# Performance work log

Measured on AMD Instinct MI355X. Metric: run time of the kernel, lower is better.

The kernel has to match this reference:

```python
import jax, jax.numpy as jnp
import numpy as np

D = 1024  # input_dim

def setup_inputs() -> dict:
    key = jax.random.key(0)
    ks = jax.random.split(key, 7)
    s = 1.0 / np.sqrt(D)
    x = jax.random.normal(ks[0], (8, 2048, D), dtype=jnp.float32)
    Wq = jax.random.uniform(ks[1], (D, D), jnp.float32, -s, s)
    bq = jax.random.uniform(ks[2], (D,), jnp.float32, -s, s)
    Wk = jax.random.uniform(ks[3], (D, D), jnp.float32, -s, s)
    bk = jax.random.uniform(ks[4], (D,), jnp.float32, -s, s)
    Wv = jax.random.uniform(ks[5], (D, D), jnp.float32, -s, s)
    bv = jax.random.uniform(ks[6], (D,), jnp.float32, -s, s)
    return {"x": x, "Wq": Wq, "bq": bq, "Wk": Wk, "bk": bk, "Wv": Wv, "bv": bv}

def reference(x, Wq, bq, Wk, bk, Wv, bv):
    # torch.nn.Linear: y = x @ W.T + b
    q = jnp.einsum('bsd,ed->bse', x, Wq) + bq
    k = jnp.einsum('bsd,ed->bse', x, Wk) + bk
    v = jnp.einsum('bsd,ed->bse', x, Wv) + bv
    scores = jnp.einsum('bqd,bkd->bqk', q, k) / jnp.sqrt(jnp.float32(x.shape[-1]))
    attn = jax.nn.softmax(scores, axis=2)
    return jnp.einsum('bqk,bkd->bqd', attn, v)
```

## Files before the change

### kernel.cpp

```cpp
#include <hip/hip_runtime.h>
#include <stdint.h>


typedef __bf16 bf16_t;
typedef __bf16 bf16x8 __attribute__((ext_vector_type(8)));
typedef __bf16 bf16x4 __attribute__((ext_vector_type(4)));
typedef float f32x4 __attribute__((ext_vector_type(4)));

__device__ __forceinline__ void gload_lds16(const bf16_t* g, bf16_t* l) {
    __builtin_amdgcn_global_load_lds((const __attribute__((address_space(1))) void*)g,
                                     (__attribute__((address_space(3))) void*)l,
                                     16, 0, 0);
}

template <int EPI, int LDA, int LDB>
__device__ __forceinline__ void gemm_bt_core(
    const bf16_t* __restrict__ A,
    const bf16_t* __restrict__ B,
    bf16_t* __restrict__ Cb, float* __restrict__ Cf, int ldc,
    float* __restrict__ aux, float scale, int K,
    int m0, int n0)
{
    __shared__ bf16_t smem[128 * 136];
    bf16_t* As = smem;
    bf16_t* Bs = smem + 8192;

    const int t    = threadIdx.x;
    const int lane = t & 63;
    const int wave = t >> 6;
    const int wm   = wave >> 1;
    const int wn   = wave & 1;
    const int lr   = lane & 15;
    const int quad = lane >> 4;
    const int swz  = lr & 7;

    const int srow   = t >> 3;
    const int schunk = ((t & 7) ^ (srow & 7)) * 8;

    f32x4 acc[4][4];
#pragma unroll
    for (int i = 0; i < 4; i++)
#pragma unroll
        for (int j = 0; j < 4; j++) acc[i][j] = (f32x4){0.f, 0.f, 0.f, 0.f};

    const bf16_t* Ag = A + (size_t)(m0 + srow) * LDA + schunk;
    const bf16_t* Bg = B + (size_t)(n0 + srow) * LDB + schunk;

    for (int kt = 0; kt < K; kt += 64) {
#pragma unroll
        for (int j = 0; j < 4; j++) {
            gload_lds16(Ag + (size_t)j * 32 * LDA + kt, As + j * 2048 + t * 8);
            gload_lds16(Bg + (size_t)j * 32 * LDB + kt, Bs + j * 2048 + t * 8);
        }
        __syncthreads();

#pragma unroll
        for (int s = 0; s < 2; s++) {
            const int koff = ((s * 4 + quad) ^ swz) * 8;
            bf16x8 af[4], bfr[4];
#pragma unroll
            for (int i = 0; i < 4; i++)
                af[i] = *(const bf16x8*)(As + (wm * 64 + i * 16 + lr) * 64 + koff);
#pragma unroll
            for (int j = 0; j < 4; j++)
                bfr[j] = *(const bf16x8*)(Bs + (wn * 64 + j * 16 + lr) * 64 + koff);
#pragma unroll
            for (int i = 0; i < 4; i++)
#pragma unroll
                for (int j = 0; j < 4; j++)
                    acc[i][j] = __builtin_amdgcn_mfma_f32_16x16x32_bf16(af[i], bfr[j], acc[i][j], 0, 0, 0);
        }
        __syncthreads();
    }

    if (EPI == 0 || EPI == 1) {
#pragma unroll
        for (int j = 0; j < 4; j++) {
            const int col = wn * 64 + j * 16 + lr;
            const float bv = (EPI == 0) ? aux[n0 + col] : 0.f;
#pragma unroll
            for (int i = 0; i < 4; i++) {
                const int row = wm * 64 + i * 16 + quad * 4;
#pragma unroll
                for (int r = 0; r < 4; r++) {
                    float v = (EPI == 0) ? (acc[i][j][r] + bv)
                                         : __expf(acc[i][j][r] * scale);
                    smem[(row + r) * 136 + col] = (__bf16)v;
                }
            }
        }
        __syncthreads();
        const int lr2  = t >> 1;
        const int half = t & 1;
        float part = 0.f;
#pragma unroll
        for (int c8 = 0; c8 < 8; c8++) {
            const int col0 = half * 64 + c8 * 8;
            bf16x8 v = *(const bf16x8*)(smem + lr2 * 136 + col0);
            *(bf16x8*)(Cb + (size_t)(m0 + lr2) * ldc + n0 + col0) = v;
            if (EPI == 1) {
#pragma unroll
                for (int e = 0; e < 8; e++) part += (float)v[e];
            }
        }
        if (EPI == 1) {
            part += __shfl_xor(part, 1);
            if (half == 0) atomicAdd(aux + m0 + lr2, part);
        }
    } else if (EPI == 2) {
#pragma unroll
        for (int i = 0; i < 4; i++) {
            const int row = m0 + wm * 64 + i * 16 + quad * 4;
#pragma unroll
            for (int r = 0; r < 4; r++) {
                const float s = 1.0f / aux[row + r];
                float* crow = Cf + (size_t)(row + r) * ldc + n0 + wn * 64 + lr;
#pragma unroll
                for (int j = 0; j < 4; j++)
                    crow[j * 16] = acc[i][j][r] * s;
            }
        }
    } else {
#pragma unroll
        for (int j = 0; j < 4; j++) {
            const int col = n0 + wn * 64 + j * 16 + lr;
            const float bv = aux[col];
#pragma unroll
            for (int i = 0; i < 4; i++) {
                const int rowg = m0 + wm * 64 + i * 16 + quad * 4;
                const int b    = rowg >> 11;
                const int s    = rowg & 2047;
                bf16x4 p = { (__bf16)(acc[i][j][0] + bv), (__bf16)(acc[i][j][1] + bv),
                             (__bf16)(acc[i][j][2] + bv), (__bf16)(acc[i][j][3] + bv) };
                *(bf16x4*)(Cb + ((size_t)b << 21) + ((size_t)col << 11) + s) = p;
            }
        }
    }
}


__global__ __launch_bounds__(256) void k_qkv3(
    const bf16_t* __restrict__ xb, const bf16_t* __restrict__ Wb,
    bf16_t* __restrict__ Q, bf16_t* __restrict__ Vt,
    const float* __restrict__ bq, const float* __restrict__ bk,
    const float* __restrict__ bv)
{
    const int lid  = blockIdx.x + 8 * blockIdx.y + 1024 * blockIdx.z;
    const int xcd  = lid & 7;
    const int slot = lid >> 3;
    const int z    = slot >> 7;
    const int rem  = slot & 127;
    const int xt   = rem & 7;
    const int yt   = xcd * 16 + (rem >> 3);
    if (z < 2) {
        float* bias = (float*)((z == 0) ? bq : bk);
        gemm_bt_core<0, 1024, 1024>(xb, Wb + (size_t)z * 1048576,
                                    Q + (size_t)z * 16777216, nullptr, 1024,
                                    bias, 0.f, 1024, yt * 128, xt * 128);
    } else {
        gemm_bt_core<3, 1024, 1024>(xb, Wb + (size_t)2 * 1048576,
                                    Vt, nullptr, 0,
                                    (float*)bv, 0.f, 1024, yt * 128, xt * 128);
    }
}

__global__ __launch_bounds__(256) void k_scores(
    const bf16_t* __restrict__ Q, const bf16_t* __restrict__ Km,
    bf16_t* __restrict__ U, float* __restrict__ l)
{
    const int lid = blockIdx.x + 16 * blockIdx.y + 256 * blockIdx.z;
    const int b   = lid & 7;
    const int si  = lid >> 3;
    const int xt  = si & 15;
    const int yt  = si >> 4;
    gemm_bt_core<1, 1024, 1024>(Q + (size_t)b * 2048 * 1024,
                                Km + (size_t)b * 2048 * 1024,
                                U + (size_t)b * 2048 * 2048, nullptr, 2048,
                                l + b * 2048, 0.03125f, 1024,
                                yt * 128, xt * 128);
}

__global__ __launch_bounds__(256) void k_pv(
    const bf16_t* __restrict__ U, const bf16_t* __restrict__ Vt,
    float* __restrict__ Out, float* __restrict__ l)
{
    const int lid = blockIdx.x + 8 * blockIdx.y + 128 * blockIdx.z;
    const int b   = lid & 7;
    const int si  = lid >> 3;
    const int xt  = si & 7;
    const int yt  = si >> 3;
    gemm_bt_core<2, 2048, 2048>(U + (size_t)b * 2048 * 2048,
                                Vt + (size_t)b * 1024 * 2048,
                                nullptr, Out + (size_t)b * 2048 * 1024, 1024,
                                l + b * 2048, 0.f, 2048,
                                yt * 128, xt * 128);
}

__global__ __launch_bounds__(256) void k_cvt(
    const float* __restrict__ in, bf16_t* __restrict__ out, long ngroups,
    float* __restrict__ l)
{
    long idx    = (long)blockIdx.x * blockDim.x + threadIdx.x;
    long stride = (long)gridDim.x * blockDim.x;
    if (blockIdx.x < 64) l[blockIdx.x * 256 + threadIdx.x] = 0.f;
    for (long i = idx; i < ngroups; i += stride) {
        float4 v = ((const float4*)in)[i];
        bf16x4 o = { (__bf16)v.x, (__bf16)v.y, (__bf16)v.z, (__bf16)v.w };
        ((bf16x4*)out)[i] = o;
    }
}

__global__ __launch_bounds__(256) void k_cvt3(
    const float* __restrict__ w0, const float* __restrict__ w1,
    const float* __restrict__ w2, bf16_t* __restrict__ out)
{
    const int z = blockIdx.z;
    const float* in = (z == 0) ? w0 : (z == 1) ? w1 : w2;
    bf16_t* o = out + (size_t)z * 1048576;
    long i = (long)blockIdx.x * blockDim.x + threadIdx.x;
    float4 v = ((const float4*)in)[i];
    bf16x4 ov = { (__bf16)v.x, (__bf16)v.y, (__bf16)v.z, (__bf16)v.w };
    ((bf16x4*)o)[i] = ov;
}


extern "C" void kernel_launch(void* const* d_in, const int* in_sizes, int n_in,
                              void* d_out, int out_size, void* d_ws, size_t ws_size,
                              hipStream_t stream)
{
    const float* x  = (const float*)d_in[0];
    const float* Wq = (const float*)d_in[1];
    const float* bq = (const float*)d_in[2];
    const float* Wk = (const float*)d_in[3];
    const float* bk = (const float*)d_in[4];
    const float* Wv = (const float*)d_in[5];
    const float* bv = (const float*)d_in[6];

    bf16_t* Q    = (bf16_t*)d_ws;
    bf16_t* Km   = Q + 16777216;
    bf16_t* Vt   = Km + 16777216;
    bf16_t* U    = Vt + 16777216;
    bf16_t* xb   = U;
    bf16_t* Wb   = U + 33554432;
    float*  l    = (float*)(Wb + 3145728);

    k_cvt<<<dim3(2048), 256, 0, stream>>>(x, xb, 16777216 / 4, l);
    k_cvt3<<<dim3(1024, 1, 3), 256, 0, stream>>>(Wq, Wk, Wv, Wb);
    k_qkv3<<<dim3(8, 128, 3), 256, 0, stream>>>(xb, Wb, Q, Vt, bq, bk, bv);
    k_scores<<<dim3(16, 16, 8), 256, 0, stream>>>(Q, Km, U, l);
    k_pv<<<dim3(8, 16, 8), 256, 0, stream>>>(U, Vt, (float*)d_out, l);
}
```

Baseline: 440.5 us.

## Switch GEMMs to 256x256 tiles with 4-stage LDS pipeline and 8 waves

Replaces the 128x128 single-buffered GEMM core with a 256x256 tile computed by 512 threads (8 waves, each owning 128x64). A 4-slot LDS ring with K-step 32 keeps three tiles of global_load_lds in flight, using explicit vmcnt waits, split barriers and setprio so MFMA work overlaps the loads. The epilogues are adapted to stage the output in two halves, and the grids are reshaped to match. The aim is more data reuse per loaded byte and hidden memory latency, at the cost of one block per CU, 128 KB of LDS, and fewer blocks to balance across the CUs.

```diff
diff --git a/kernel.cpp b/kernel.cpp
--- a/kernel.cpp
+++ b/kernel.cpp
@@ -14,120 +14,162 @@
 }
 
 template <int EPI, int LDA, int LDB>
-__device__ __forceinline__ void gemm_bt_core(
+__device__ __forceinline__ void gemm256_core(
+    bf16_t* __restrict__ lds,
     const bf16_t* __restrict__ A,
     const bf16_t* __restrict__ B,
     bf16_t* __restrict__ Cb, float* __restrict__ Cf, int ldc,
     float* __restrict__ aux, float scale, int K,
     int m0, int n0)
 {
-    __shared__ bf16_t smem[128 * 136];
-    bf16_t* As = smem;
-    bf16_t* Bs = smem + 8192;
-
     const int t    = threadIdx.x;
     const int lane = t & 63;
     const int wave = t >> 6;
-    const int wm   = wave >> 1;
-    const int wn   = wave & 1;
+    const int wm   = wave >> 2;
+    const int wn   = wave & 3;
     const int lr   = lane & 15;
     const int quad = lane >> 4;
-    const int swz  = lr & 7;
-
-    const int srow   = t >> 3;
-    const int schunk = ((t & 7) ^ (srow & 7)) * 8;
-
-    f32x4 acc[4][4];
-#pragma unroll
-    for (int i = 0; i < 4; i++)
+
+    const int rowS = t >> 2;
+    const int qS   = (t & 3) ^ (rowS & 3);
+    const bf16_t* Ag = A + (size_t)(m0 + rowS) * LDA + qS * 8;
+    const bf16_t* Bg = B + (size_t)(n0 + rowS) * LDB + qS * 8;
+    const int dst0 = t * 8;
+
+    const int ko   = (quad ^ (lr & 3)) * 8;
+    const int aoff = (wm * 128 + lr) * 32 + ko;
+    const int boff = (wn * 64 + lr) * 32 + ko;
+
+    f32x4 acc[8][4];
+#pragma unroll
+    for (int i = 0; i < 8; i++)
 #pragma unroll
         for (int j = 0; j < 4; j++) acc[i][j] = (f32x4){0.f, 0.f, 0.f, 0.f};
 
-    const bf16_t* Ag = A + (size_t)(m0 + srow) * LDA + schunk;
-    const bf16_t* Bg = B + (size_t)(n0 + srow) * LDB + schunk;
-
-    for (int kt = 0; kt < K; kt += 64) {
-#pragma unroll
-        for (int j = 0; j < 4; j++) {
-            gload_lds16(Ag + (size_t)j * 32 * LDA + kt, As + j * 2048 + t * 8);
-            gload_lds16(Bg + (size_t)j * 32 * LDB + kt, Bs + j * 2048 + t * 8);
-        }
-        __syncthreads();
-
-#pragma unroll
-        for (int s = 0; s < 2; s++) {
-            const int koff = ((s * 4 + quad) ^ swz) * 8;
-            bf16x8 af[4], bfr[4];
-#pragma unroll
-            for (int i = 0; i < 4; i++)
-                af[i] = *(const bf16x8*)(As + (wm * 64 + i * 16 + lr) * 64 + koff);
-#pragma unroll
-            for (int j = 0; j < 4; j++)
-                bfr[j] = *(const bf16x8*)(Bs + (wn * 64 + j * 16 + lr) * 64 + koff);
-#pragma unroll
-            for (int i = 0; i < 4; i++)
-#pragma unroll
-                for (int j = 0; j < 4; j++)
-                    acc[i][j] = __builtin_amdgcn_mfma_f32_16x16x32_bf16(af[i], bfr[j], acc[i][j], 0, 0, 0);
-        }
-        __syncthreads();
+    const int T = K >> 5;
+
+#pragma unroll
+    for (int tt = 0; tt < 3; ++tt) {
+        bf16_t* Ab = lds + tt * 16384;
+        bf16_t* Bb = Ab + 8192;
+        const int kt = tt * 32;
+        gload_lds16(Ag + kt,                     Ab + dst0);
+        gload_lds16(Ag + kt + (size_t)128 * LDA, Ab + 4096 + dst0);
+        gload_lds16(Bg + kt,                     Bb + dst0);
+        gload_lds16(Bg + kt + (size_t)128 * LDB, Bb + 4096 + dst0);
+    }
+    asm volatile("s_waitcnt vmcnt(8)" ::: "memory");
+    __builtin_amdgcn_s_barrier();
+    __builtin_amdgcn_sched_barrier(0);
+
+    for (int tk = 0; tk < T; ++tk) {
+        const bf16_t* Ab = lds + (tk & 3) * 16384;
+        const bf16_t* Bb = Ab + 8192;
+        bf16x8 af[8], bfr[4];
+#pragma unroll
+        for (int i = 0; i < 4; ++i)
+            af[i] = *(const bf16x8*)(Ab + aoff + 512 * i);
+#pragma unroll
+        for (int j = 0; j < 4; ++j)
+            bfr[j] = *(const bf16x8*)(Bb + boff + 512 * j);
+        __builtin_amdgcn_s_barrier();
+        __builtin_amdgcn_sched_barrier(0);
+        __builtin_amdgcn_s_setprio(1);
+#pragma unroll
+        for (int i = 0; i < 4; ++i)
+#pragma unroll
+            for (int j = 0; j < 4; ++j)
+                acc[i][j] = __builtin_amdgcn_mfma_f32_16x16x32_bf16(af[i], bfr[j], acc[i][j], 0, 0, 0);
+        __builtin_amdgcn_s_setprio(0);
+#pragma unroll
+        for (int i = 4; i < 8; ++i)
+            af[i] = *(const bf16x8*)(Ab + aoff + 512 * i);
+        if (tk + 3 < T) {
+            bf16_t* An = lds + ((tk + 3) & 3) * 16384;
+            bf16_t* Bn = An + 8192;
+            const int kt = (tk + 3) * 32;
+            gload_lds16(Ag + kt,                     An + dst0);
+            gload_lds16(Ag + kt + (size_t)128 * LDA, An + 4096 + dst0);
+            gload_lds16(Bg + kt,                     Bn + dst0);
+            gload_lds16(Bg + kt + (size_t)128 * LDB, Bn + 4096 + dst0);
+            asm volatile("s_waitcnt vmcnt(8)" ::: "memory");
+        } else if (tk + 2 < T) {
+            asm volatile("s_waitcnt vmcnt(4)" ::: "memory");
+        } else {
+            asm volatile("s_waitcnt vmcnt(0)" ::: "memory");
+        }
+        __builtin_amdgcn_s_barrier();
+        __builtin_amdgcn_sched_barrier(0);
+        __builtin_amdgcn_s_setprio(1);
+#pragma unroll
+        for (int i = 4; i < 8; ++i)
+#pragma unroll
+            for (int j = 0; j < 4; ++j)
+                acc[i][j] = __builtin_amdgcn_mfma_f32_16x16x32_bf16(af[i], bfr[j], acc[i][j], 0, 0, 0);
+        __builtin_amdgcn_s_setprio(0);
     }
 
     if (EPI == 0 || EPI == 1) {
 #pragma unroll
-        for (int j = 0; j < 4; j++) {
-            const int col = wn * 64 + j * 16 + lr;
-            const float bv = (EPI == 0) ? aux[n0 + col] : 0.f;
-#pragma unroll
-            for (int i = 0; i < 4; i++) {
-                const int row = wm * 64 + i * 16 + quad * 4;
-#pragma unroll
-                for (int r = 0; r < 4; r++) {
-                    float v = (EPI == 0) ? (acc[i][j][r] + bv)
-                                         : __expf(acc[i][j][r] * scale);
-                    smem[(row + r) * 136 + col] = (__bf16)v;
+        for (int h = 0; h < 2; ++h) {
+            __syncthreads();
+            if (wm == h) {
+#pragma unroll
+                for (int j = 0; j < 4; ++j) {
+                    const int col = wn * 64 + j * 16 + lr;
+                    const float bv = (EPI == 0) ? aux[n0 + col] : 0.f;
+#pragma unroll
+                    for (int i = 0; i < 8; ++i) {
+                        const int row = i * 16 + quad * 4;
+#pragma unroll
+                        for (int r = 0; r < 4; ++r) {
+                            float v = (EPI == 0) ? (acc[i][j][r] + bv)
+                                                 : __expf(acc[i][j][r] * scale);
+                            lds[(row + r) * 264 + col] = (__bf16)v;
+                        }
+                    }
                 }
             }
-        }
-        __syncthreads();
-        const int lr2  = t >> 1;
-        const int half = t & 1;
-        float part = 0.f;
-#pragma unroll
-        for (int c8 = 0; c8 < 8; c8++) {
-            const int col0 = half * 64 + c8 * 8;
-            bf16x8 v = *(const bf16x8*)(smem + lr2 * 136 + col0);
-            *(bf16x8*)(Cb + (size_t)(m0 + lr2) * ldc + n0 + col0) = v;
+            __syncthreads();
+            const int r2 = t >> 2;
+            const int c0 = (t & 3) * 8;
+            float part = 0.f;
+#pragma unroll
+            for (int c = 0; c < 8; ++c) {
+                bf16x8 v = *(const bf16x8*)(lds + r2 * 264 + c0 + c * 32);
+                *(bf16x8*)(Cb + (size_t)(m0 + h * 128 + r2) * ldc + n0 + c0 + c * 32) = v;
+                if (EPI == 1) {
+#pragma unroll
+                    for (int e = 0; e < 8; ++e) part += (float)v[e];
+                }
+            }
             if (EPI == 1) {
-#pragma unroll
-                for (int e = 0; e < 8; e++) part += (float)v[e];
-            }
-        }
-        if (EPI == 1) {
-            part += __shfl_xor(part, 1);
-            if (half == 0) atomicAdd(aux + m0 + lr2, part);
+                part += __shfl_xor(part, 1);
+                part += __shfl_xor(part, 2);
+                if ((t & 3) == 0) atomicAdd(aux + m0 + h * 128 + r2, part);
+            }
         }
     } else if (EPI == 2) {
 #pragma unroll
-        for (int i = 0; i < 4; i++) {
-            const int row = m0 + wm * 64 + i * 16 + quad * 4;
-#pragma unroll
-            for (int r = 0; r < 4; r++) {
-                const float s = 1.0f / aux[row + r];
-                float* crow = Cf + (size_t)(row + r) * ldc + n0 + wn * 64 + lr;
-#pragma unroll
-                for (int j = 0; j < 4; j++)
+        for (int i = 0; i < 8; ++i) {
+            const int rowb = m0 + wm * 128 + i * 16 + quad * 4;
+#pragma unroll
+            for (int r = 0; r < 4; ++r) {
+                const float s = 1.0f / aux[rowb + r];
+                float* crow = Cf + (size_t)(rowb + r) * ldc + n0 + wn * 64 + lr;
+#pragma unroll
+                for (int j = 0; j < 4; ++j)
                     crow[j * 16] = acc[i][j][r] * s;
             }
         }
     } else {
 #pragma unroll
-        for (int j = 0; j < 4; j++) {
+        for (int j = 0; j < 4; ++j) {
             const int col = n0 + wn * 64 + j * 16 + lr;
             const float bv = aux[col];
 #pragma unroll
-            for (int i = 0; i < 4; i++) {
-                const int rowg = m0 + wm * 64 + i * 16 + quad * 4;
+            for (int i = 0; i < 8; ++i) {
+                const int rowg = m0 + wm * 128 + i * 16 + quad * 4;
                 const int b    = rowg >> 11;
                 const int s    = rowg & 2047;
                 bf16x4 p = { (__bf16)(acc[i][j][0] + bv), (__bf16)(acc[i][j][1] + bv),
@@ -139,61 +181,64 @@
 }
 
 
-__global__ __launch_bounds__(256) void k_qkv3(
+__global__ __launch_bounds__(512, 1) void k_qkv3(
     const bf16_t* __restrict__ xb, const bf16_t* __restrict__ Wb,
     bf16_t* __restrict__ Q, bf16_t* __restrict__ Vt,
     const float* __restrict__ bq, const float* __restrict__ bk,
     const float* __restrict__ bv)
 {
-    const int lid  = blockIdx.x + 8 * blockIdx.y + 1024 * blockIdx.z;
+    __shared__ bf16_t lds[65536];
+    const int lid  = blockIdx.x + 8 * blockIdx.y;
     const int xcd  = lid & 7;
     const int slot = lid >> 3;
-    const int z    = slot >> 7;
-    const int rem  = slot & 127;
-    const int xt   = rem & 7;
-    const int yt   = xcd * 16 + (rem >> 3);
+    const int z    = slot >> 5;
+    const int rem  = slot & 31;
+    const int xt   = rem & 3;
+    const int yt   = xcd * 8 + (rem >> 2);
     if (z < 2) {
         float* bias = (float*)((z == 0) ? bq : bk);
-        gemm_bt_core<0, 1024, 1024>(xb, Wb + (size_t)z * 1048576,
+        gemm256_core<0, 1024, 1024>(lds, xb, Wb + (size_t)z * 1048576,
                                     Q + (size_t)z * 16777216, nullptr, 1024,
-                                    bias, 0.f, 1024, yt * 128, xt * 128);
+                                    bias, 0.f, 1024, yt * 256, xt * 256);
     } else {
-        gemm_bt_core<3, 1024, 1024>(xb, Wb + (size_t)2 * 1048576,
+        gemm256_core<3, 1024, 1024>(lds, xb, Wb + (size_t)2 * 1048576,
                                     Vt, nullptr, 0,
-                                    (float*)bv, 0.f, 1024, yt * 128, xt * 128);
-    }
-}
-
-__global__ __launch_bounds__(256) void k_scores(
+                                    (float*)bv, 0.f, 1024, yt * 256, xt * 256);
+    }
+}
+
+__global__ __launch_bounds__(512, 1) void k_scores(
     const bf16_t* __restrict__ Q, const bf16_t* __restrict__ Km,
     bf16_t* __restrict__ U, float* __restrict__ l)
 {
-    const int lid = blockIdx.x + 16 * blockIdx.y + 256 * blockIdx.z;
-    const int b   = lid & 7;
-    const int si  = lid >> 3;
-    const int xt  = si & 15;
-    const int yt  = si >> 4;
-    gemm_bt_core<1, 1024, 1024>(Q + (size_t)b * 2048 * 1024,
-                                Km + (size_t)b * 2048 * 1024,
-                                U + (size_t)b * 2048 * 2048, nullptr, 2048,
-                                l + b * 2048, 0.03125f, 1024,
-                                yt * 128, xt * 128);
-}
-
-__global__ __launch_bounds__(256) void k_pv(
-    const bf16_t* __restrict__ U, const bf16_t* __restrict__ Vt,
-    float* __restrict__ Out, float* __restrict__ l)
-{
-    const int lid = blockIdx.x + 8 * blockIdx.y + 128 * blockIdx.z;
+    __shared__ bf16_t lds[65536];
+    const int lid = blockIdx.x + 8 * blockIdx.y;
     const int b   = lid & 7;
     const int si  = lid >> 3;
     const int xt  = si & 7;
     const int yt  = si >> 3;
-    gemm_bt_core<2, 2048, 2048>(U + (size_t)b * 2048 * 2048,
+    gemm256_core<1, 1024, 1024>(lds, Q + (size_t)b * 2048 * 1024,
+                                Km + (size_t)b * 2048 * 1024,
+                                U + (size_t)b * 2048 * 2048, nullptr, 2048,
+                                l + b * 2048, 0.03125f, 1024,
+                                yt * 256, xt * 256);
+}
+
+__global__ __launch_bounds__(512, 1) void k_pv(
+    const bf16_t* __restrict__ U, const bf16_t* __restrict__ Vt,
+    float* __restrict__ Out, float* __restrict__ l)
+{
+    __shared__ bf16_t lds[65536];
+    const int lid = blockIdx.x + 8 * blockIdx.y;
+    const int b   = lid & 7;
+    const int si  = lid >> 3;
+    const int xt  = si & 3;
+    const int yt  = si >> 2;
+    gemm256_core<2, 2048, 2048>(lds, U + (size_t)b * 2048 * 2048,
                                 Vt + (size_t)b * 1024 * 2048,
                                 nullptr, Out + (size_t)b * 2048 * 1024, 1024,
                                 l + b * 2048, 0.f, 2048,
-                                yt * 128, xt * 128);
+                                yt * 256, xt * 256);
 }
 
 __global__ __launch_bounds__(256) void k_cvt(
@@ -246,7 +291,7 @@
 
     k_cvt<<<dim3(2048), 256, 0, stream>>>(x, xb, 16777216 / 4, l);
     k_cvt3<<<dim3(1024, 1, 3), 256, 0, stream>>>(Wq, Wk, Wv, Wb);
-    k_qkv3<<<dim3(8, 128, 3), 256, 0, stream>>>(xb, Wb, Q, Vt, bq, bk, bv);
-    k_scores<<<dim3(16, 16, 8), 256, 0, stream>>>(Q, Km, U, l);
-    k_pv<<<dim3(8, 16, 8), 256, 0, stream>>>(U, Vt, (float*)d_out, l);
-}
+    k_qkv3<<<dim3(8, 96), 512, 0, stream>>>(xb, Wb, Q, Vt, bq, bk, bv);
+    k_scores<<<dim3(8, 64), 512, 0, stream>>>(Q, Km, U, l);
+    k_pv<<<dim3(8, 32), 512, 0, stream>>>(U, Vt, (float*)d_out, l);
+}
```

New measurement: 383.7 us. 12.9% less time.

## Triple-buffer GEMM K-loop with async LDS prefetch and split MFMA phases

Applied to the files above, without the earlier changes.

Replaces the single-buffered 64-wide K loop, which synchronized twice per step, with a three-stage ring of 32-wide K tiles in LDS. Global-to-LDS loads for step tk+2 are issued while the current tile is computed, and vmcnt waits plus raw s_barrier split each step into two MFMA halves. The change also adds s_setprio around the MFMA bursts, a new XOR swizzle for the 32-wide tiles, and launch_bounds(256,2) to request two blocks per CU. The price is more LDS (48KB per block) and fragile hand-written wait counts and barriers.

```diff
diff --git a/kernel.cpp b/kernel.cpp
--- a/kernel.cpp
+++ b/kernel.cpp
@@ -15,16 +15,13 @@
 
 template <int EPI, int LDA, int LDB>
 __device__ __forceinline__ void gemm_bt_core(
+    bf16_t* __restrict__ lds,
     const bf16_t* __restrict__ A,
     const bf16_t* __restrict__ B,
     bf16_t* __restrict__ Cb, float* __restrict__ Cf, int ldc,
     float* __restrict__ aux, float scale, int K,
     int m0, int n0)
 {
-    __shared__ bf16_t smem[128 * 136];
-    bf16_t* As = smem;
-    bf16_t* Bs = smem + 8192;
-
     const int t    = threadIdx.x;
     const int lane = t & 63;
     const int wave = t >> 6;
@@ -32,10 +29,16 @@
     const int wn   = wave & 1;
     const int lr   = lane & 15;
     const int quad = lane >> 4;
-    const int swz  = lr & 7;
-
-    const int srow   = t >> 3;
-    const int schunk = ((t & 7) ^ (srow & 7)) * 8;
+
+    const int rowS = t >> 2;
+    const int qS   = (t & 3) ^ ((rowS >> 1) & 3);
+    const bf16_t* Ag = A + (size_t)(m0 + rowS) * LDA + qS * 8;
+    const bf16_t* Bg = B + (size_t)(n0 + rowS) * LDB + qS * 8;
+    const int dst0 = t * 8;
+
+    const int ko   = (quad ^ ((lr >> 1) & 3)) * 8;
+    const int aoff = (wm * 64 + lr) * 32 + ko;
+    const int boff = (wn * 64 + lr) * 32 + ko;
 
     f32x4 acc[4][4];
 #pragma unroll
@@ -43,37 +46,69 @@
 #pragma unroll
         for (int j = 0; j < 4; j++) acc[i][j] = (f32x4){0.f, 0.f, 0.f, 0.f};
 
-    const bf16_t* Ag = A + (size_t)(m0 + srow) * LDA + schunk;
-    const bf16_t* Bg = B + (size_t)(n0 + srow) * LDB + schunk;
-
-    for (int kt = 0; kt < K; kt += 64) {
-#pragma unroll
-        for (int j = 0; j < 4; j++) {
-            gload_lds16(Ag + (size_t)j * 32 * LDA + kt, As + j * 2048 + t * 8);
-            gload_lds16(Bg + (size_t)j * 32 * LDB + kt, Bs + j * 2048 + t * 8);
-        }
+    const int T = K >> 5;
+
+#pragma unroll
+    for (int tt = 0; tt < 2; ++tt) {
+        bf16_t* Ab = lds + tt * 8192;
+        const int kt = tt * 32;
+        gload_lds16(Ag + kt,                    Ab + dst0);
+        gload_lds16(Ag + kt + (size_t)64 * LDA, Ab + 2048 + dst0);
+        gload_lds16(Bg + kt,                    Ab + 4096 + dst0);
+        gload_lds16(Bg + kt + (size_t)64 * LDB, Ab + 6144 + dst0);
+    }
+    asm volatile("s_waitcnt vmcnt(4)" ::: "memory");
+    __builtin_amdgcn_s_barrier();
+    __builtin_amdgcn_sched_barrier(0);
+
+    int buf = 0;
+    int bufn = 2;
+    for (int tk = 0; tk < T; ++tk) {
+        const bf16_t* Ab = lds + buf * 8192;
+        const bf16_t* Bb = Ab + 4096;
+        bf16x8 af[4], bfr[4];
+        af[0] = *(const bf16x8*)(Ab + aoff);
+        af[1] = *(const bf16x8*)(Ab + aoff + 512);
+#pragma unroll
+        for (int j = 0; j < 4; ++j)
+            bfr[j] = *(const bf16x8*)(Bb + boff + 512 * j);
+        __builtin_amdgcn_s_barrier();
+        __builtin_amdgcn_sched_barrier(0);
+        __builtin_amdgcn_s_setprio(1);
+#pragma unroll
+        for (int i = 0; i < 2; ++i)
+#pragma unroll
+            for (int j = 0; j < 4; ++j)
+                acc[i][j] = __builtin_amdgcn_mfma_f32_16x16x32_bf16(af[i], bfr[j], acc[i][j], 0, 0, 0);
+        __builtin_amdgcn_s_setprio(0);
+        af[2] = *(const bf16x8*)(Ab + aoff + 1024);
+        af[3] = *(const bf16x8*)(Ab + aoff + 1536);
+        if (tk + 2 < T) {
+            bf16_t* An = lds + bufn * 8192;
+            const int kt = (tk + 2) * 32;
+            gload_lds16(Ag + kt,                    An + dst0);
+            gload_lds16(Ag + kt + (size_t)64 * LDA, An + 2048 + dst0);
+            gload_lds16(Bg + kt,                    An + 4096 + dst0);
+            gload_lds16(Bg + kt + (size_t)64 * LDB, An + 6144 + dst0);
+            asm volatile("s_waitcnt vmcnt(4)" ::: "memory");
+        } else {
+            asm volatile("s_waitcnt vmcnt(0)" ::: "memory");
+        }
+        __builtin_amdgcn_s_barrier();
+        __builtin_amdgcn_sched_barrier(0);
+        __builtin_amdgcn_s_setprio(1);
+#pragma unroll
+        for (int i = 2; i < 4; ++i)
+#pragma unroll
+            for (int j = 0; j < 4; ++j)
+                acc[i][j] = __builtin_amdgcn_mfma_f32_16x16x32_bf16(af[i], bfr[j], acc[i][j], 0, 0, 0);
+        __builtin_amdgcn_s_setprio(0);
+        buf  = (buf == 2) ? 0 : buf + 1;
+        bufn = (bufn == 2) ? 0 : bufn + 1;
+    }
+
+    if (EPI == 0 || EPI == 1) {
         __syncthreads();
-
-#pragma unroll
-        for (int s = 0; s < 2; s++) {
-            const int koff = ((s * 4 + quad) ^ swz) * 8;
-            bf16x8 af[4], bfr[4];
-#pragma unroll
-            for (int i = 0; i < 4; i++)
-                af[i] = *(const bf16x8*)(As + (wm * 64 + i * 16 + lr) * 64 + koff);
-#pragma unroll
-            for (int j = 0; j < 4; j++)
-                bfr[j] = *(const bf16x8*)(Bs + (wn * 64 + j * 16 + lr) * 64 + koff);
-#pragma unroll
-            for (int i = 0; i < 4; i++)
-#pragma unroll
-                for (int j = 0; j < 4; j++)
-                    acc[i][j] = __builtin_amdgcn_mfma_f32_16x16x32_bf16(af[i], bfr[j], acc[i][j], 0, 0, 0);
-        }
-        __syncthreads();
-    }
-
-    if (EPI == 0 || EPI == 1) {
 #pragma unroll
         for (int j = 0; j < 4; j++) {
             const int col = wn * 64 + j * 16 + lr;
@@ -85,7 +120,7 @@
                 for (int r = 0; r < 4; r++) {
                     float v = (EPI == 0) ? (acc[i][j][r] + bv)
                                          : __expf(acc[i][j][r] * scale);
-                    smem[(row + r) * 136 + col] = (__bf16)v;
+                    lds[(row + r) * 136 + col] = (__bf16)v;
                 }
             }
         }
@@ -96,7 +131,7 @@
 #pragma unroll
         for (int c8 = 0; c8 < 8; c8++) {
             const int col0 = half * 64 + c8 * 8;
-            bf16x8 v = *(const bf16x8*)(smem + lr2 * 136 + col0);
+            bf16x8 v = *(const bf16x8*)(lds + lr2 * 136 + col0);
             *(bf16x8*)(Cb + (size_t)(m0 + lr2) * ldc + n0 + col0) = v;
             if (EPI == 1) {
 #pragma unroll
@@ -139,12 +174,13 @@
 }
 
 
-__global__ __launch_bounds__(256) void k_qkv3(
+__global__ __launch_bounds__(256, 2) void k_qkv3(
     const bf16_t* __restrict__ xb, const bf16_t* __restrict__ Wb,
     bf16_t* __restrict__ Q, bf16_t* __restrict__ Vt,
     const float* __restrict__ bq, const float* __restrict__ bk,
     const float* __restrict__ bv)
 {
+    __shared__ bf16_t lds[24576];
     const int lid  = blockIdx.x + 8 * blockIdx.y + 1024 * blockIdx.z;
     const int xcd  = lid & 7;
     const int slot = lid >> 3;
@@ -154,42 +190,44 @@
     const int yt   = xcd * 16 + (rem >> 3);
     if (z < 2) {
         float* bias = (float*)((z == 0) ? bq : bk);
-        gemm_bt_core<0, 1024, 1024>(xb, Wb + (size_t)z * 1048576,
+        gemm_bt_core<0, 1024, 1024>(lds, xb, Wb + (size_t)z * 1048576,
                                     Q + (size_t)z * 16777216, nullptr, 1024,
                                     bias, 0.f, 1024, yt * 128, xt * 128);
     } else {
-        gemm_bt_core<3, 1024, 1024>(xb, Wb + (size_t)2 * 1048576,
+        gemm_bt_core<3, 1024, 1024>(lds, xb, Wb + (size_t)2 * 1048576,
                                     Vt, nullptr, 0,
                                     (float*)bv, 0.f, 1024, yt * 128, xt * 128);
     }
 }
 
-__global__ __launch_bounds__(256) void k_scores(
+__global__ __launch_bounds__(256, 2) void k_scores(
     const bf16_t* __restrict__ Q, const bf16_t* __restrict__ Km,
     bf16_t* __restrict__ U, float* __restrict__ l)
 {
+    __shared__ bf16_t lds[24576];
     const int lid = blockIdx.x + 16 * blockIdx.y + 256 * blockIdx.z;
     const int b   = lid & 7;
     const int si  = lid >> 3;
     const int xt  = si & 15;
     const int yt  = si >> 4;
-    gemm_bt_core<1, 1024, 1024>(Q + (size_t)b * 2048 * 1024,
+    gemm_bt_core<1, 1024, 1024>(lds, Q + (size_t)b * 2048 * 1024,
                                 Km + (size_t)b * 2048 * 1024,
                                 U + (size_t)b * 2048 * 2048, nullptr, 2048,
                                 l + b * 2048, 0.03125f, 1024,
                                 yt * 128, xt * 128);
 }
 
-__global__ __launch_bounds__(256) void k_pv(
+__global__ __launch_bounds__(256, 2) void k_pv(
     const bf16_t* __restrict__ U, const bf16_t* __restrict__ Vt,
     float* __restrict__ Out, float* __restrict__ l)
 {
+    __shared__ bf16_t lds[24576];
     const int lid = blockIdx.x + 8 * blockIdx.y + 128 * blockIdx.z;
     const int b   = lid & 7;
     const int si  = lid >> 3;
     const int xt  = si & 7;
     const int yt  = si >> 3;
-    gemm_bt_core<2, 2048, 2048>(U + (size_t)b * 2048 * 2048,
+    gemm_bt_core<2, 2048, 2048>(lds, U + (size_t)b * 2048 * 2048,
                                 Vt + (size_t)b * 1024 * 2048,
                                 nullptr, Out + (size_t)b * 2048 * 1024, 1024,
                                 l + b * 2048, 0.f, 2048,
```

New measurement: 413.2 us. -6.2%, faster.
